# Kernel tuning notes

Measured on AMD Instinct MI355X. Metric: run time of the kernel, lower is better.

## Reference

```python
import jax, jax.numpy as jnp
import numpy as np

N, D, E = 8192, 768, 262144
DI, DS, DCONV, DTR = 1536, 16, 4, 48  # d_inner=2*768, d_state, d_conv, dt_rank=ceil(768/16)


def setup_inputs() -> dict:
    key = jax.random.key(0)
    ks = jax.random.split(key, 12)
    s = 0.02
    return {
        "node_feats": jax.random.normal(ks[0], (N, D), jnp.float32),
        "timestamps": jax.random.randint(ks[1], (N,), 0, 1_000_000, dtype=jnp.int32),
        "edge_index": jax.random.randint(ks[2], (2, E), 0, N, dtype=jnp.int32),
        "W_in": jax.random.normal(ks[3], (D, 2 * DI), jnp.float32) * s,
        "conv_w": jax.random.normal(ks[4], (DI, DCONV), jnp.float32) * s,
        "conv_b": jnp.zeros((DI,), jnp.float32),
        "W_xproj": jax.random.normal(ks[5], (DI, DTR + 2 * DS), jnp.float32) * s,
        "W_dt": jax.random.normal(ks[6], (DTR, DI), jnp.float32) * s,
        "b_dt": jnp.zeros((DI,), jnp.float32),
        "A_log": jnp.log(jnp.broadcast_to(jnp.arange(1, DS + 1, dtype=jnp.float32), (DI, DS))),
        "D_param": jnp.ones((DI,), jnp.float32),
        "W_out": jax.random.normal(ks[7], (DI, D), jnp.float32) * s,
        "Wg": jax.random.normal(ks[8], (3, D, D), jnp.float32) * s,
        "bg": jnp.zeros((3, D), jnp.float32),
        "W_c": jax.random.normal(ks[9], (D, 1), jnp.float32) * s,
        "b_c": jnp.zeros((1,), jnp.float32),
    }


def _mamba(x, W_in, conv_w, conv_b, W_xproj, W_dt, b_dt, A_log, D_param, W_out):
    # x: [L, D]
    L = x.shape[0]
    xz = x @ W_in                      # [L, 2*DI]
    xi, z = xz[:, :DI], xz[:, DI:]
    # causal depthwise conv1d, kernel DCONV
    xp = jnp.pad(xi, ((DCONV - 1, 0), (0, 0)))
    xc = conv_b
    for k in range(DCONV):
        xc = xc + xp[k:k + L] * conv_w[:, k]
    u = jax.nn.silu(xc)                # [L, DI]
    dbc = u @ W_xproj                  # [L, DTR+2*DS]
    delta = jax.nn.softplus(dbc[:, :DTR] @ W_dt + b_dt)  # [L, DI]
    B = dbc[:, DTR:DTR + DS]           # [L, DS]
    C = dbc[:, DTR + DS:]              # [L, DS]
    A = -jnp.exp(A_log)                # [DI, DS]

    def step(h, inp):
        dt, Bt, Ct, ut = inp
        dA = jnp.exp(dt[:, None] * A)                    # [DI, DS]
        h = h * dA + (dt * ut)[:, None] * Bt[None, :]    # [DI, DS]
        return h, (h * Ct[None, :]).sum(-1)              # y_t: [DI]

    h0 = jnp.zeros((DI, DS), x.dtype)
    _, y = jax.lax.scan(step, h0, (delta, B, C, u))      # [L, DI]
    y = (y + u * D_param) * jax.nn.silu(z)
    return y @ W_out                   # [L, D]


def reference(node_feats, timestamps, edge_index, W_in, conv_w, conv_b,
              W_xproj, W_dt, b_dt, A_log, D_param, W_out, Wg, bg, W_c, b_c):
    src, dst = edge_index[0], edge_index[1]
    # degree norms (DGL GraphConv norm='both', clamp min 1)
    ones = jnp.ones((E,), node_feats.dtype)
    out_deg = jnp.clip(jax.ops.segment_sum(ones, src, num_segments=N), 1.0)
    in_deg = jnp.clip(jax.ops.segment_sum(ones, dst, num_segments=N), 1.0)
    norm_s = out_deg ** -0.5
    norm_d = in_deg ** -0.5

    sorted_idx = jnp.argsort(timestamps)
    seq = node_feats[sorted_idx]
    h = _mamba(seq, W_in, conv_w, conv_b, W_xproj, W_dt, b_dt, A_log, D_param, W_out)
    # NOTE: original code feeds sorted-order features to GCN without unsorting (replicated).
    for i in range(3):
        x = h * norm_s[:, None]
        m = jax.ops.segment_sum(x[src], dst, num_segments=N) * norm_d[:, None]
        h = jax.nn.gelu(m @ Wg[i] + bg[i], approximate=False)
    causal = jax.nn.sigmoid(h @ W_c + b_c).squeeze(-1)   # [N]
    graph_feat = h.mean(axis=0)                          # [D]
    return graph_feat, causal, causal > 0.7
```

## Files before the change

kernel.cpp:

```cpp
#include <hip/hip_runtime.h>
#include <math.h>

#define NN 8192
#define DF 768
#define NE_ 262144
#define DIM 1536
#define DSN 16
#define NCH 128
#define CL  64
#define CT  64

typedef short short8 __attribute__((ext_vector_type(8)));
typedef float f32x4 __attribute__((ext_vector_type(4)));
typedef unsigned short us4 __attribute__((ext_vector_type(4)));

__device__ __forceinline__ float bf2f(unsigned short u){
  unsigned int v = ((unsigned int)u) << 16; float f; __builtin_memcpy(&f, &v, 4); return f;
}
__device__ __forceinline__ unsigned short f2bf(float f){
  unsigned int x; __builtin_memcpy(&x, &f, 4);
  x += 0x7fffu + ((x >> 16) & 1u);
  return (unsigned short)(x >> 16);
}
#define EXP2RAW(x) __builtin_amdgcn_exp2f(x)
#define LOG2E 1.44269504088896f
#define LN2   0.69314718055995f
#define H8SCALE 64.f
__device__ __forceinline__ float sigmoidf_(float x){
  return 1.f/(1.f + EXP2RAW(-x*LOG2E));
}
__device__ __forceinline__ float softplusf_(float v){
  if (v > 20.f) return v;
  return LN2 * __log2f(1.f + EXP2RAW(v*LOG2E));
}

__device__ __forceinline__ unsigned char f2fp8(float v){
  float y = v * H8SCALE;
#if __has_builtin(__builtin_amdgcn_cvt_pk_fp8_f32)
  return (unsigned char)(__builtin_amdgcn_cvt_pk_fp8_f32(y, y, 0, false) & 0xff);
#else
  unsigned int u; __builtin_memcpy(&u, &y, 4);
  unsigned char s = (unsigned char)((u >> 24) & 0x80);
  float a = fabsf(y);
  if (a >= 448.f) return (unsigned char)(s | 0x7E);
  if (a < 0x1p-10f) return s;
  unsigned int ab = u & 0x7fffffffu;
  int ef = (int)(ab >> 23) - 127;
  int qe = ef - 3; if (qe < -9) qe = -9;
  float q; { unsigned int qb = (unsigned int)(qe + 127) << 23; __builtin_memcpy(&q, &qb, 4); }
  float n = rintf(a / q);
  float m = n * q;
  unsigned int mb; __builtin_memcpy(&mb, &m, 4);
  int E = (int)(mb >> 23) - 127 + 7;
  unsigned char out;
  if (E <= 0) out = (unsigned char)rintf(m * 512.f);
  else        out = (unsigned char)((E << 3) | ((mb >> 20) & 7));
  return (unsigned char)(s | out);
#endif
}
__device__ __forceinline__ float fp8bits(unsigned int b){
  unsigned int t = ((b & 0x80u) << 24) | ((b & 0x7fu) << 20);
  float f; __builtin_memcpy(&f, &t, 4); return f;
}

__device__ __forceinline__ void gl_lds16(const unsigned short* g, unsigned short* l){
  __builtin_amdgcn_global_load_lds(
      (const __attribute__((address_space(1))) unsigned int*)g,
      (__attribute__((address_space(3))) unsigned int*)l,
      16, 0, 0);
}

__global__ __launch_bounds__(256) void k_prep(
    const float* __restrict__ W_in, const float* __restrict__ W_xproj,
    const float* __restrict__ W_dt, const float* __restrict__ W_out,
    const float* __restrict__ Wg,
    unsigned short* __restrict__ WinT, unsigned short* __restrict__ WxT,
    unsigned short* __restrict__ WdtT, unsigned short* __restrict__ WoutT,
    unsigned short* __restrict__ WgT,
    int* __restrict__ pos, int* __restrict__ degS, float* __restrict__ outv)
{
  int b = blockIdx.x;
  int tid = threadIdx.x;
  if (b >= 1368){
    if (b < 1400)       pos[(b-1368)*256 + tid] = 0;
    else if (b < 1464)  degS[(b-1400)*256 + tid] = 0;
    else { outv[tid] = 0.f; outv[256+tid] = 0.f; outv[512+tid] = 0.f; }
    return;
  }
  const float* in; unsigned short* out; int K, N, Kp, Np, kt, nt;
  if (b < 576){        in = W_in;    out = WinT;  K = 768;  N = 3072; Kp = 768;  Np = 3072;
                       kt = b / 48;  nt = b % 48; }
  else if (b < 624){   int l = b - 576;
                       in = W_xproj; out = WxT;   K = 1536; N = 80;   Kp = 1536; Np = 128;
                       kt = l >> 1;  nt = l & 1; }
  else if (b < 648){   int l = b - 624;
                       in = W_dt;    out = WdtT;  K = 48;   N = 1536; Kp = 64;   Np = 1536;
                       kt = 0;       nt = l; }
  else if (b < 936){   int l = b - 648;
                       in = W_out;   out = WoutT; K = 1536; N = 768;  Kp = 1536; Np = 768;
                       kt = l / 12;  nt = l % 12; }
  else {               int l = b - 936;
                       int g = l / 144; int r = l % 144;
                       in = Wg + (size_t)g*768*768; out = WgT + (size_t)g*768*768;
                       K = 768; N = 768; Kp = 768; Np = 768;
                       kt = r / 12;  nt = r % 12; }
  int k0 = kt*64, n0 = nt*64;
  __shared__ float tl[64][65];
  int ln = tid & 63;
  int lk = tid >> 6;
  #pragma unroll
  for (int kk = lk; kk < 64; kk += 4){
    int gk = k0 + kk, gn = n0 + ln;
    float v = (gk < K && gn < N) ? in[(size_t)gk*N + gn] : 0.f;
    tl[kk][ln] = v;
  }
  __syncthreads();
  #pragma unroll
  for (int nn = lk; nn < 64; nn += 4){
    int gn2 = n0 + nn, gk2 = k0 + ln;
    if (gn2 < Np && gk2 < Kp)
      out[(size_t)gn2*Kp + gk2] = f2bf(tl[ln][nn]);
  }
}

__global__ __launch_bounds__(256) void k_rank_deg(const int* __restrict__ ts, int* __restrict__ pos,
                                                  const int* __restrict__ esrc, const int* __restrict__ edst,
                                                  int* __restrict__ degS, int* __restrict__ degD){
  int b = blockIdx.x;
  if (b < 1024){
    __shared__ int sT[256];
    int ic = b & 31, jc = b >> 5;
    int i = ic*256 + threadIdx.x;
    int my = ts[i];
    int c0 = jc*256;
    sT[threadIdx.x] = ts[c0 + threadIdx.x];
    __syncthreads();
    int r = 0;
    #pragma unroll 8
    for (int j = 0; j < 256; j++){
      int t = sT[j]; int jj = c0 + j;
      r += (t < my || (t == my && jj < i)) ? 1 : 0;
    }
    atomicAdd(&pos[i], r);
  } else {
    int e = (b-1024)*256 + threadIdx.x;
    atomicAdd(&degS[esrc[e]], 1); atomicAdd(&degD[edst[e]], 1);
  }
}

__global__ __launch_bounds__(1024) void k_graphfix(const int* __restrict__ degS, const int* __restrict__ degD,
                                                   float* __restrict__ normS, float* __restrict__ normD,
                                                   int* __restrict__ row_ptr, int* __restrict__ cursor){
  int b = blockIdx.x;
  int tid = threadIdx.x;
  if (b < 8){
    int i = b*1024 + tid;
    normS[i] = rsqrtf(fmaxf((float)degS[i], 1.f));
    normD[i] = rsqrtf(fmaxf((float)degD[i], 1.f));
    return;
  }
  __shared__ int sp[1024];
  int base = tid*8;
  int loc[8]; int s = 0;
  #pragma unroll
  for (int j = 0; j < 8; j++){ loc[j] = degD[base+j]; s += loc[j]; }
  sp[tid] = s; __syncthreads();
  for (int o = 1; o < 1024; o <<= 1){
    int v = (tid >= o) ? sp[tid-o] : 0; __syncthreads();
    sp[tid] += v; __syncthreads();
  }
  int run = sp[tid] - s;
  #pragma unroll
  for (int j = 0; j < 8; j++){ row_ptr[base+j] = run; cursor[base+j] = run; run += loc[j]; }
  if (tid == 1023) row_ptr[NN] = sp[1023];
}

__global__ __launch_bounds__(256) void k_scatter(const float* __restrict__ nf, const int* __restrict__ pos,
                                                 unsigned short* __restrict__ seq,
                                                 const int* __restrict__ esrc, const int* __restrict__ edst,
                                                 int* __restrict__ cursor, int* __restrict__ csr_src){
  int b = blockIdx.x;
  if (b < NN){
    int p = pos[b];
    const float* src = nf + (size_t)b*DF;
    unsigned short* dst = seq + (size_t)p*DF;
    for (int j = threadIdx.x; j < DF/4; j += 256){
      f32x4 v = *(const f32x4*)&src[j*4];
      us4 o = { f2bf(v.x), f2bf(v.y), f2bf(v.z), f2bf(v.w) };
      *(us4*)&dst[j*4] = o;
    }
  } else {
    int e = (b-NN)*256 + threadIdx.x;
    int d = edst[e];
    int p = atomicAdd(&cursor[d], 1);
    csr_src[p] = esrc[e];
  }
}

template<int EPI>
__global__ __launch_bounds__(256) void k_gemm(
    const unsigned short* __restrict__ A, const unsigned short* __restrict__ B,
    int N, int K, int lda, int ldb,
    float* __restrict__ outF, int ldoF,
    unsigned short* __restrict__ outB, int ldoB,
    const float* __restrict__ bias,
    unsigned short* __restrict__ out2,
    unsigned char* __restrict__ outQ,
    const float* __restrict__ nrmS)
{
  __shared__ unsigned short sA[2][128*32];
  __shared__ unsigned short sB[2][128*32];
  int tid = threadIdx.x;
  int tnc = N >> 7;
  int nwg = gridDim.x;
  int bid = blockIdx.x;
  int swz = (nwg & 7) ? bid : ((bid & 7)*(nwg >> 3) + (bid >> 3));
  int bm = (swz / tnc) << 7;
  int bn = (swz % tnc) << 7;
  int wv = tid >> 6, lane = tid & 63;
  int wm = wv >> 1, wn = wv & 1;
  int l15 = lane & 15, l4 = lane >> 4;

  f32x4 acc[4][4];
  #pragma unroll
  for (int i = 0; i < 4; i++)
    #pragma unroll
    for (int j = 0; j < 4; j++)
      acc[i][j] = (f32x4){0.f,0.f,0.f,0.f};

  int r0 = (wv*2)*16 + (lane >> 2);
  int r1 = r0 + 16;
  int cc = (lane & 3)*8;
  const unsigned short* gA0 = A + (size_t)(bm + r0)*lda + cc;
  const unsigned short* gA1 = A + (size_t)(bm + r1)*lda + cc;
  const unsigned short* gB0 = B + (size_t)(bn + r0)*ldb + cc;
  const unsigned short* gB1 = B + (size_t)(bn + r1)*ldb + cc;
  unsigned short* lA0 = &sA[0][(size_t)(wv*2)*512];
  unsigned short* lA1 = &sA[1][(size_t)(wv*2)*512];
  unsigned short* lB0 = &sB[0][(size_t)(wv*2)*512];
  unsigned short* lB1 = &sB[1][(size_t)(wv*2)*512];

  for (int k0 = 0; k0 < K; k0 += 64){
    __syncthreads();
    gl_lds16(gA0 + k0,      lA0);
    gl_lds16(gA1 + k0,      lA0 + 512);
    gl_lds16(gA0 + k0 + 32, lA1);
    gl_lds16(gA1 + k0 + 32, lA1 + 512);
    gl_lds16(gB0 + k0,      lB0);
    gl_lds16(gB1 + k0,      lB0 + 512);
    gl_lds16(gB0 + k0 + 32, lB1);
    gl_lds16(gB1 + k0 + 32, lB1 + 512);
    __syncthreads();
    #pragma unroll
    for (int h = 0; h < 2; h++){
      short8 af[4], bf_[4];
      #pragma unroll
      for (int i = 0; i < 4; i++){
        af[i]  = *(const short8*)&sA[h][(wm*64 + i*16 + l15)*32 + l4*8];
        bf_[i] = *(const short8*)&sB[h][(wn*64 + i*16 + l15)*32 + l4*8];
      }
      #pragma unroll
      for (int i = 0; i < 4; i++)
        #pragma unroll
        for (int j = 0; j < 4; j++)
          acc[i][j] = __builtin_amdgcn_mfma_f32_16x16x32_bf16(af[i], bf_[j], acc[i][j], 0, 0, 0);
    }
  }

  #pragma unroll
  for (int i = 0; i < 4; i++)
    #pragma unroll
    for (int j = 0; j < 4; j++)
      #pragma unroll
      for (int rr = 0; rr < 4; rr++){
        int row = bm + wm*64 + i*16 + l4*4 + rr;
        int col = bn + wn*64 + j*16 + l15;
        float v = acc[i][j][rr];
        if (EPI == 0){
          outB[(size_t)row*ldoB + col] = f2bf(v);
        } else if (EPI == 1){
          outF[(size_t)row*ldoF + col] = v;
          if (col < 64) out2[(size_t)row*64 + col] = (col < 48) ? f2bf(v) : (unsigned short)0;
        } else if (EPI == 2){
          outB[(size_t)row*ldoB + col] = f2bf(softplusf_(v + bias[col]));
        } else if (EPI == 3){
          v += bias[col];
          float g = 0.5f*v*(1.f + erff(v*0.70710678118f));
          outB[(size_t)row*ldoB + col] = f2bf(g);
        } else if (EPI == 4){
          v += bias[col];
          float g = 0.5f*v*(1.f + erff(v*0.70710678118f));
          outQ[(size_t)row*ldoB + col] = f2fp8(g * nrmS[row]);
        } else {
          outQ[(size_t)row*ldoB + col] = f2fp8(v * nrmS[row]);
        }
      }
}

__global__ __launch_bounds__(256) void k_conv_silu(const unsigned short* __restrict__ xz,
                                                   const float* __restrict__ conv_w,
                                                   const float* __restrict__ conv_b,
                                                   unsigned short* __restrict__ u){
  int c = blockIdx.x*256 + threadIdx.x;
  int t0 = blockIdx.y*CT;
  float w0 = conv_w[c*4], w1 = conv_w[c*4+1], w2 = conv_w[c*4+2], w3 = conv_w[c*4+3];
  float bb = conv_b[c];
  const unsigned short* xp = xz + c;
  float x0 = (t0 >= 3) ? bf2f(xp[(size_t)(t0-3)*3072]) : 0.f;
  float x1 = (t0 >= 2) ? bf2f(xp[(size_t)(t0-2)*3072]) : 0.f;
  float x2 = (t0 >= 1) ? bf2f(xp[(size_t)(t0-1)*3072]) : 0.f;
  unsigned short* up = u + (size_t)t0*DIM + c;
  for (int r0 = 0; r0 < CT; r0 += 8){
    unsigned short xb[8];
    #pragma unroll
    for (int j = 0; j < 8; j++) xb[j] = xp[(size_t)(t0+r0+j)*3072];
    #pragma unroll
    for (int j = 0; j < 8; j++){
      float x3 = bf2f(xb[j]);
      float acc = bb + x0*w0 + x1*w1 + x2*w2 + x3*w3;
      up[(r0+j)*DIM] = f2bf(acc * sigmoidf_(acc));
      x0 = x1; x1 = x2; x2 = x3;
    }
  }
}

__device__ __forceinline__ void pow_tree(float e1, float dA[16]){
  float e2 = e1*e1, e4 = e2*e2, e8 = e4*e4;
  dA[0]=e1;      dA[1]=e2;      dA[2]=e2*e1;   dA[3]=e4;
  dA[4]=e4*e1;   dA[5]=e4*e2;   dA[6]=e4*dA[2];dA[7]=e8;
  dA[8]=e8*e1;   dA[9]=e8*e2;   dA[10]=e8*dA[2];dA[11]=e8*e4;
  dA[12]=e8*dA[4];dA[13]=e8*dA[5];dA[14]=e8*dA[6];dA[15]=e8*e8;
}

__global__ __launch_bounds__(256) void k_scanA(
    const unsigned short* __restrict__ delta, const unsigned short* __restrict__ u,
    const float* __restrict__ dbc, const float* __restrict__ A_log,
    const float* __restrict__ D_param,
    float* __restrict__ hend, float* __restrict__ aprod,
    unsigned short* __restrict__ ylocal)
{
  __shared__ float sBC[CL][32];
  int tid = threadIdx.x;
  int c = blockIdx.x*256 + tid;
  int k = blockIdx.y;
  float al2[16];
  #pragma unroll
  for (int s = 0; s < 16; s++) al2[s] = -expf(A_log[(size_t)c*16 + s]) * LOG2E;
  bool fast = true;
  #pragma unroll
  for (int s = 1; s < 16; s++)
    fast = fast && (fabsf(al2[s] - (float)(s+1)*al2[0]) <= 1e-4f*fabsf(al2[s]));
  float Dc = D_param[c];
  float h[16];
  #pragma unroll
  for (int s = 0; s < 16; s++) h[s] = 0.f;
  float sdt = 0.f;
  for (int idx = tid; idx < CL*32; idx += 256){
    int t = idx >> 5, j = idx & 31;
    sBC[t][j] = dbc[(size_t)(k*CL + t)*128 + 48 + j];
  }
  __syncthreads();
  const unsigned short* dp = delta + (size_t)k*CL*DIM + c;
  const unsigned short* up = u + (size_t)k*CL*DIM + c;
  unsigned short* yp = ylocal + (size_t)k*CL*DIM + c;
  if (fast){
    for (int t0 = 0; t0 < CL; t0 += 8){
      unsigned short dtb[8], uub[8];
      #pragma unroll
      for (int j = 0; j < 8; j++){
        dtb[j] = dp[(t0+j)*DIM];
        uub[j] = up[(t0+j)*DIM];
      }
      #pragma unroll
      for (int j = 0; j < 8; j++){
        int t = t0 + j;
        float dt = bf2f(dtb[j]), uu = bf2f(uub[j]);
        f32x4 Bv[4], Cv[4];
        #pragma unroll
        for (int q = 0; q < 4; q++){
          Bv[q] = *(const f32x4*)&sBC[t][q*4];
          Cv[q] = *(const f32x4*)&sBC[t][16 + q*4];
        }
        float dtu = dt*uu;
        sdt += dt;
        float dA[16];
        pow_tree(EXP2RAW(dt*al2[0]), dA);
        float ap[4] = {0.f,0.f,0.f,0.f};
        #pragma unroll
        for (int s = 0; s < 16; s++){
          h[s] = h[s]*dA[s] + dtu*Bv[s>>2][s&3];
          ap[s>>2] += h[s]*Cv[s>>2][s&3];
        }
        float accv = (ap[0]+ap[1]) + (ap[2]+ap[3]);
        yp[t*DIM] = f2bf(accv + uu*Dc);
      }
    }
  } else {
    unsigned short dtn = dp[0], uun = up[0];
    #pragma unroll 2
    for (int t = 0; t < CL; t++){
      float dt = bf2f(dtn), uu = bf2f(uun);
      int tn = (t+1 < CL) ? t+1 : t;
      dtn = dp[tn*DIM]; uun = up[tn*DIM];
      f32x4 Bv[4], Cv[4];
      #pragma unroll
      for (int q = 0; q < 4; q++){
        Bv[q] = *(const f32x4*)&sBC[t][q*4];
        Cv[q] = *(const f32x4*)&sBC[t][16 + q*4];
      }
      float dtu = dt*uu;
      sdt += dt;
      float ap[4] = {0.f,0.f,0.f,0.f};
      #pragma unroll
      for (int s = 0; s < 16; s++){
        float dA = EXP2RAW(dt*al2[s]);
        h[s] = h[s]*dA + dtu*Bv[s>>2][s&3];
        ap[s>>2] += h[s]*Cv[s>>2][s&3];
      }
      float accv = (ap[0]+ap[1]) + (ap[2]+ap[3]);
      yp[t*DIM] = f2bf(accv + uu*Dc);
    }
  }
  size_t base = ((size_t)k*DIM + c)*16;
  #pragma unroll
  for (int s = 0; s < 16; s += 4){
    *(f32x4*)&hend[base+s]  = (f32x4){h[s],h[s+1],h[s+2],h[s+3]};
    *(f32x4*)&aprod[base+s] = (f32x4){EXP2RAW(al2[s]*sdt),EXP2RAW(al2[s+1]*sdt),
                                      EXP2RAW(al2[s+2]*sdt),EXP2RAW(al2[s+3]*sdt)};
  }
}

__global__ __launch_bounds__(256) void k_scanB(float* __restrict__ hend, const float* __restrict__ aprod){
  int i = blockIdx.x*256 + threadIdx.x;
  float H = 0.f;
  for (int k0 = 0; k0 < NCH; k0 += 8){
    float e[8], ap[8];
    #pragma unroll
    for (int j = 0; j < 8; j++){
      size_t o = (size_t)(k0+j)*DIM*16 + i;
      e[j] = hend[o]; ap[j] = aprod[o];
    }
    #pragma unroll
    for (int j = 0; j < 8; j++){
      size_t o = (size_t)(k0+j)*DIM*16 + i;
      hend[o] = H;
      H = e[j] + ap[j]*H;
    }
  }
}

__global__ __launch_bounds__(256) void k_scanCorr(
    const unsigned short* __restrict__ delta, const unsigned short* __restrict__ xz,
    const float* __restrict__ dbc, const float* __restrict__ A_log,
    const float* __restrict__ hin, unsigned short* __restrict__ y)
{
  __shared__ float sC[CL][16];
  int tid = threadIdx.x;
  int c = blockIdx.x*256 + tid;
  int k = blockIdx.y;
  float al2[16];
  #pragma unroll
  for (int s = 0; s < 16; s++) al2[s] = -expf(A_log[(size_t)c*16 + s]) * LOG2E;
  bool fast = true;
  #pragma unroll
  for (int s = 1; s < 16; s++)
    fast = fast && (fabsf(al2[s] - (float)(s+1)*al2[0]) <= 1e-4f*fabsf(al2[s]));
  float alSlow = al2[0];
  #pragma unroll
  for (int s = 1; s < 16; s++) alSlow = fmaxf(alSlow, al2[s]);
  float Hin[16];
  size_t base = ((size_t)k*DIM + c)*16;
  #pragma unroll
  for (int s = 0; s < 16; s += 4){
    f32x4 v = *(const f32x4*)&hin[base+s];
    Hin[s] = v.x; Hin[s+1] = v.y; Hin[s+2] = v.z; Hin[s+3] = v.w;
  }
  for (int idx = tid; idx < CL*16; idx += 256){
    int t = idx >> 4, j = idx & 15;
    sC[t][j] = dbc[(size_t)(k*CL + t)*128 + 64 + j];
  }
  __syncthreads();
  const unsigned short* dp = delta + (size_t)k*CL*DIM + c;
  const unsigned short* zp = xz + (size_t)k*CL*3072 + 1536 + c;
  unsigned short* yp = y + (size_t)k*CL*DIM + c;
  float cum = 0.f;
  int t = 0;
  if (fast){
    bool done = false;
    for (int t0 = 0; t0 < CL && !done; t0 += 8){
      unsigned short dtb[8], zzb[8], ylb[8];
      #pragma unroll
      for (int j = 0; j < 8; j++){
        dtb[j] = dp[(t0+j)*DIM];
        zzb[j] = zp[(t0+j)*3072];
        ylb[j] = yp[(t0+j)*DIM];
      }
      #pragma unroll
      for (int j = 0; j < 8; j++){
        float dt = bf2f(dtb[j]);
        cum += dt;
        float e1 = EXP2RAW(cum*al2[0]);
        if (e1 < 0x1p-33f){ t = t0 + j; done = true; break; }
        float dA[16];
        pow_tree(e1, dA);
        f32x4 Cv[4];
        #pragma unroll
        for (int q = 0; q < 4; q++) Cv[q] = *(const f32x4*)&sC[t0+j][q*4];
        float ap[4] = {0.f,0.f,0.f,0.f};
        #pragma unroll
        for (int s = 0; s < 16; s++)
          ap[s>>2] += Hin[s]*dA[s]*Cv[s>>2][s&3];
        float corr = (ap[0]+ap[1]) + (ap[2]+ap[3]);
        float yl = bf2f(ylb[j]);
        float zz = bf2f(zzb[j]);
        yp[(t0+j)*DIM] = f2bf((yl + corr) * (zz * sigmoidf_(zz)));
      }
      if (!done) t = t0 + 8;
    }
  } else {
    for (; t < CL; t++){
      float dt = bf2f(dp[t*DIM]);
      cum += dt;
      if (EXP2RAW(cum*alSlow) < 0x1p-33f) break;
      f32x4 Cv[4];
      #pragma unroll
      for (int q = 0; q < 4; q++) Cv[q] = *(const f32x4*)&sC[t][q*4];
      float ap[4] = {0.f,0.f,0.f,0.f};
      #pragma unroll
      for (int s = 0; s < 16; s++)
        ap[s>>2] += Hin[s]*EXP2RAW(cum*al2[s])*Cv[s>>2][s&3];
      float corr = (ap[0]+ap[1]) + (ap[2]+ap[3]);
      float yl = bf2f(yp[t*DIM]);
      float zz = bf2f(zp[t*3072]);
      float yv = (yl + corr) * (zz * sigmoidf_(zz));
      yp[t*DIM] = f2bf(yv);
    }
  }
  for (; t + 7 < CL; t += 8){
    unsigned short zzb[8], ylb[8];
    #pragma unroll
    for (int j = 0; j < 8; j++){
      ylb[j] = yp[(t+j)*DIM];
      zzb[j] = zp[(t+j)*3072];
    }
    #pragma unroll
    for (int j = 0; j < 8; j++){
      float yl = bf2f(ylb[j]);
      float zz = bf2f(zzb[j]);
      yp[(t+j)*DIM] = f2bf(yl * (zz * sigmoidf_(zz)));
    }
  }
  for (; t < CL; t++){
    float yl = bf2f(yp[t*DIM]);
    float zz = bf2f(zp[t*3072]);
    yp[t*DIM] = f2bf(yl * (zz * sigmoidf_(zz)));
  }
}

__global__ __launch_bounds__(192) void k_aggregate(
    const unsigned char* __restrict__ hq, const int* __restrict__ row_ptr,
    const int* __restrict__ csr_src, const float* __restrict__ normD,
    unsigned short* __restrict__ m)
{
  int d = blockIdx.x; int tid = threadIdx.x;
  int e0 = row_ptr[d], e1 = row_ptr[d+1];
  float a0 = 0.f, a1 = 0.f, a2 = 0.f, a3 = 0.f;
#if __has_builtin(__builtin_amdgcn_cvt_f32_fp8)
  int e = e0;
  for (; e + 7 < e1; e += 8){
    int sx[8];
    #pragma unroll
    for (int j = 0; j < 8; j++) sx[j] = csr_src[e+j];
    unsigned int w[8];
    #pragma unroll
    for (int j = 0; j < 8; j++) w[j] = *((const unsigned int*)(hq + (size_t)sx[j]*DF) + tid);
    a0 += (__builtin_amdgcn_cvt_f32_fp8(w[0], 0) + __builtin_amdgcn_cvt_f32_fp8(w[1], 0))
        + (__builtin_amdgcn_cvt_f32_fp8(w[2], 0) + __builtin_amdgcn_cvt_f32_fp8(w[3], 0));
    a1 += (__builtin_amdgcn_cvt_f32_fp8(w[0], 1) + __builtin_amdgcn_cvt_f32_fp8(w[1], 1))
        + (__builtin_amdgcn_cvt_f32_fp8(w[2], 1) + __builtin_amdgcn_cvt_f32_fp8(w[3], 1));
    a2 += (__builtin_amdgcn_cvt_f32_fp8(w[0], 2) + __builtin_amdgcn_cvt_f32_fp8(w[1], 2))
        + (__builtin_amdgcn_cvt_f32_fp8(w[2], 2) + __builtin_amdgcn_cvt_f32_fp8(w[3], 2));
    a3 += (__builtin_amdgcn_cvt_f32_fp8(w[0], 3) + __builtin_amdgcn_cvt_f32_fp8(w[1], 3))
        + (__builtin_amdgcn_cvt_f32_fp8(w[2], 3) + __builtin_amdgcn_cvt_f32_fp8(w[3], 3));
    a0 += (__builtin_amdgcn_cvt_f32_fp8(w[4], 0) + __builtin_amdgcn_cvt_f32_fp8(w[5], 0))
        + (__builtin_amdgcn_cvt_f32_fp8(w[6], 0) + __builtin_amdgcn_cvt_f32_fp8(w[7], 0));
    a1 += (__builtin_amdgcn_cvt_f32_fp8(w[4], 1) + __builtin_amdgcn_cvt_f32_fp8(w[5], 1))
        + (__builtin_amdgcn_cvt_f32_fp8(w[6], 1) + __builtin_amdgcn_cvt_f32_fp8(w[7], 1));
    a2 += (__builtin_amdgcn_cvt_f32_fp8(w[4], 2) + __builtin_amdgcn_cvt_f32_fp8(w[5], 2))
        + (__builtin_amdgcn_cvt_f32_fp8(w[6], 2) + __builtin_amdgcn_cvt_f32_fp8(w[7], 2));
    a3 += (__builtin_amdgcn_cvt_f32_fp8(w[4], 3) + __builtin_amdgcn_cvt_f32_fp8(w[5], 3))
        + (__builtin_amdgcn_cvt_f32_fp8(w[6], 3) + __builtin_amdgcn_cvt_f32_fp8(w[7], 3));
  }
  for (; e + 3 < e1; e += 4){
    int s0 = csr_src[e],   s1 = csr_src[e+1];
    int s2 = csr_src[e+2], s3 = csr_src[e+3];
    unsigned int w0 = *((const unsigned int*)(hq + (size_t)s0*DF) + tid);
    unsigned int w1 = *((const unsigned int*)(hq + (size_t)s1*DF) + tid);
    unsigned int w2 = *((const unsigned int*)(hq + (size_t)s2*DF) + tid);
    unsigned int w3 = *((const unsigned int*)(hq + (size_t)s3*DF) + tid);
    a0 += (__builtin_amdgcn_cvt_f32_fp8(w0, 0) + __builtin_amdgcn_cvt_f32_fp8(w1, 0))
        + (__builtin_amdgcn_cvt_f32_fp8(w2, 0) + __builtin_amdgcn_cvt_f32_fp8(w3, 0));
    a1 += (__builtin_amdgcn_cvt_f32_fp8(w0, 1) + __builtin_amdgcn_cvt_f32_fp8(w1, 1))
        + (__builtin_amdgcn_cvt_f32_fp8(w2, 1) + __builtin_amdgcn_cvt_f32_fp8(w3, 1));
    a2 += (__builtin_amdgcn_cvt_f32_fp8(w0, 2) + __builtin_amdgcn_cvt_f32_fp8(w1, 2))
        + (__builtin_amdgcn_cvt_f32_fp8(w2, 2) + __builtin_amdgcn_cvt_f32_fp8(w3, 2));
    a3 += (__builtin_amdgcn_cvt_f32_fp8(w0, 3) + __builtin_amdgcn_cvt_f32_fp8(w1, 3))
        + (__builtin_amdgcn_cvt_f32_fp8(w2, 3) + __builtin_amdgcn_cvt_f32_fp8(w3, 3));
  }
  for (; e < e1; e++){
    int s0 = csr_src[e];
    unsigned int w0 = *((const unsigned int*)(hq + (size_t)s0*DF) + tid);
    a0 += __builtin_amdgcn_cvt_f32_fp8(w0, 0);
    a1 += __builtin_amdgcn_cvt_f32_fp8(w0, 1);
    a2 += __builtin_amdgcn_cvt_f32_fp8(w0, 2);
    a3 += __builtin_amdgcn_cvt_f32_fp8(w0, 3);
  }
  float nd = normD[d] * (1.f/H8SCALE);
#else
  for (int e = e0; e < e1; e++){
    int sI = csr_src[e];
    unsigned int w = *((const unsigned int*)(hq + (size_t)sI*DF) + tid);
    a0 += fp8bits(w & 255u);
    a1 += fp8bits((w >> 8) & 255u);
    a2 += fp8bits((w >> 16) & 255u);
    a3 += fp8bits(w >> 24);
  }
  float nd = normD[d] * 0x1p+114f;
#endif
  uint2 o;
  o.x = (unsigned int)f2bf(a0*nd) | ((unsigned int)f2bf(a1*nd) << 16);
  o.y = (unsigned int)f2bf(a2*nd) | ((unsigned int)f2bf(a3*nd) << 16);
  *((uint2*)(m + (size_t)d*DF) + tid) = o;
}

__global__ __launch_bounds__(256) void k_final(const unsigned short* __restrict__ h,
                                               const float* __restrict__ W_c,
                                               const float* __restrict__ b_c,
                                               float* __restrict__ out){
  int b = blockIdx.x;
  if (b < 2048){
    int wv = threadIdx.x >> 6, lane = threadIdx.x & 63;
    int r = b*4 + wv;
    float s = 0.f;
    #pragma unroll
    for (int j = 0; j < 12; j++){
      int cidx = lane + 64*j;
      s += bf2f(h[(size_t)r*DF + cidx]) * W_c[cidx];
    }
    s += __shfl_xor(s, 32); s += __shfl_xor(s, 16); s += __shfl_xor(s, 8);
    s += __shfl_xor(s, 4);  s += __shfl_xor(s, 2);  s += __shfl_xor(s, 1);
    if (lane == 0){
      float a = s + b_c[0];
      float cz = 1.f/(1.f + expf(-a));
      out[DF + r] = cz;
      out[DF + NN + r] = (cz > 0.7f) ? 1.f : 0.f;
    }
  } else {
    int g = b - 2048;
    int col = (g % 3)*256 + threadIdx.x;
    int r0 = (g / 3)*32;
    float s = 0.f;
    for (int rb = 0; rb < 32; rb += 8){
      unsigned short hb[8];
      #pragma unroll
      for (int j = 0; j < 8; j++) hb[j] = h[(size_t)(r0+rb+j)*DF + col];
      #pragma unroll
      for (int j = 0; j < 8; j++) s += bf2f(hb[j]);
    }
    atomicAdd(&out[col], s * (1.f/8192.f));
  }
}

extern "C" void kernel_launch(void* const* d_in, const int* in_sizes, int n_in,
                              void* d_out, int out_size, void* d_ws, size_t ws_size,
                              hipStream_t stream) {
  const float* node_feats = (const float*)d_in[0];
  const int*   timestamps = (const int*)d_in[1];
  const int*   ei         = (const int*)d_in[2];
  const int*   e_src = ei;
  const int*   e_dst = ei + NE_;
  const float* W_in    = (const float*)d_in[3];
  const float* conv_w  = (const float*)d_in[4];
  const float* conv_b  = (const float*)d_in[5];
  const float* W_xproj = (const float*)d_in[6];
  const float* W_dt    = (const float*)d_in[7];
  const float* b_dt    = (const float*)d_in[8];
  const float* A_log   = (const float*)d_in[9];
  const float* D_param = (const float*)d_in[10];
  const float* W_out   = (const float*)d_in[11];
  const float* Wg      = (const float*)d_in[12];
  const float* bg      = (const float*)d_in[13];
  const float* W_c     = (const float*)d_in[14];
  const float* b_c     = (const float*)d_in[15];
  float* out = (float*)d_out;

  char* ws = (char*)d_ws;
  size_t off = 0;
  auto alloc = [&](size_t bytes) -> char* {
    char* p = ws + off; off += (bytes + 255) & ~(size_t)255; return p;
  };
  unsigned short* WinT   = (unsigned short*)alloc((size_t)3072*768*2);
  unsigned short* WxT    = (unsigned short*)alloc((size_t)128*1536*2);
  unsigned short* WdtT   = (unsigned short*)alloc((size_t)1536*64*2);
  unsigned short* WoutT  = (unsigned short*)alloc((size_t)768*1536*2);
  unsigned short* WgT    = (unsigned short*)alloc((size_t)3*768*768*2);
  unsigned short* seq    = (unsigned short*)alloc((size_t)NN*DF*2);
  unsigned short* xz     = (unsigned short*)alloc((size_t)NN*3072*2);
  unsigned short* ubuf   = (unsigned short*)alloc((size_t)NN*DIM*2);
  float*          dbc    = (float*)alloc((size_t)NN*128*4);
  unsigned short* dt48   = (unsigned short*)alloc((size_t)NN*64*2);
  unsigned short* deltaB = (unsigned short*)alloc((size_t)NN*DIM*2);
  unsigned short* ybuf   = (unsigned short*)alloc((size_t)NN*DIM*2);
  unsigned short* hbuf   = (unsigned short*)alloc((size_t)NN*DF*2);
  unsigned short* mbuf   = (unsigned short*)alloc((size_t)NN*DF*2);
  unsigned char*  hq     = (unsigned char*)alloc((size_t)NN*DF);
  int*   pos    = (int*)alloc((size_t)NN*4);
  int*   degS   = (int*)alloc((size_t)2*NN*4);
  int*   degD   = degS + NN;
  float* normS  = (float*)alloc((size_t)NN*4);
  float* normD  = (float*)alloc((size_t)NN*4);
  int*   rowp   = (int*)alloc((size_t)(NN+1)*4);
  int*   cursor = (int*)alloc((size_t)NN*4);
  int*   csr    = (int*)alloc((size_t)NE_*4);

  float* hend  = (float*)seq;
  float* aprod = (float*)mbuf;

  k_prep<<<1465, 256, 0, stream>>>(W_in, W_xproj, W_dt, W_out, Wg,
                                   WinT, WxT, WdtT, WoutT, WgT,
                                   pos, degS, out);
  k_rank_deg<<<2048, 256, 0, stream>>>(timestamps, pos, e_src, e_dst, degS, degD);
  k_graphfix<<<9, 1024, 0, stream>>>(degS, degD, normS, normD, rowp, cursor);
  k_scatter<<<NN + 1024, 256, 0, stream>>>(node_feats, pos, seq, e_src, e_dst, cursor, csr);

  k_gemm<0><<<64*24, 256, 0, stream>>>(seq, WinT, 3072, 768, 768, 768,
                                       nullptr, 0, xz, 3072, nullptr, nullptr, nullptr, nullptr);
  k_conv_silu<<<dim3(6, NN/CT), 256, 0, stream>>>(xz, conv_w, conv_b, ubuf);
  k_gemm<1><<<64*1, 256, 0, stream>>>(ubuf, WxT, 128, 1536, 1536, 1536,
                                      dbc, 128, nullptr, 0, nullptr, dt48, nullptr, nullptr);
  k_gemm<2><<<64*12, 256, 0, stream>>>(dt48, WdtT, 1536, 64, 64, 64,
                                       nullptr, 0, deltaB, 1536, b_dt, nullptr, nullptr, nullptr);
  k_scanA<<<dim3(DIM/256, NCH), 256, 0, stream>>>(deltaB, ubuf, dbc, A_log, D_param, hend, aprod, ybuf);
  k_scanB<<<96, 256, 0, stream>>>(hend, aprod);
  k_scanCorr<<<dim3(DIM/256, NCH), 256, 0, stream>>>(deltaB, xz, dbc, A_log, hend, ybuf);
  k_gemm<5><<<64*6, 256, 0, stream>>>(ybuf, WoutT, 768, 1536, 1536, 1536,
                                      nullptr, 0, nullptr, 768, nullptr, nullptr, hq, normS);
  k_aggregate<<<NN, 192, 0, stream>>>(hq, rowp, csr, normD, mbuf);
  k_gemm<4><<<64*6, 256, 0, stream>>>(mbuf, WgT, 768, 768, 768, 768,
                                      nullptr, 0, nullptr, 768, bg, nullptr, hq, normS);
  k_aggregate<<<NN, 192, 0, stream>>>(hq, rowp, csr, normD, mbuf);
  k_gemm<4><<<64*6, 256, 0, stream>>>(mbuf, WgT + (size_t)768*768, 768, 768, 768, 768,
                                      nullptr, 0, nullptr, 768, bg + 768, nullptr, hq, normS);
  k_aggregate<<<NN, 192, 0, stream>>>(hq, rowp, csr, normD, mbuf);
  k_gemm<3><<<64*6, 256, 0, stream>>>(mbuf, WgT + (size_t)2*768*768, 768, 768, 768, 768,
                                      nullptr, 0, hbuf, 768, bg + 2*768, nullptr, nullptr, nullptr);
  k_final<<<2816, 256, 0, stream>>>(hbuf, W_c, b_c, out);
}
```

Baseline: 452.9 us.

## Double-buffer GEMM LDS tiles to overlap global loads with MFMA compute

The GEMM main loop now uses the two LDS halves as a ping-pong buffer over 32-wide K steps. It issues the global-to-LDS loads for the next slice before computing on the current one, where the old loop loaded both halves and then computed. This aims to hide global load latency behind MFMA work. In exchange it runs twice as many iterations, each with a barrier, and does half as much MFMA work per iteration. Correctness depends on the direct-to-LDS loads being complete at the single barrier each step.

```diff
diff --git a/kernel.cpp b/kernel.cpp
--- a/kernel.cpp
+++ b/kernel.cpp
@@ -235,36 +235,39 @@
   const unsigned short* gA1 = A + (size_t)(bm + r1)*lda + cc;
   const unsigned short* gB0 = B + (size_t)(bn + r0)*ldb + cc;
   const unsigned short* gB1 = B + (size_t)(bn + r1)*ldb + cc;
-  unsigned short* lA0 = &sA[0][(size_t)(wv*2)*512];
-  unsigned short* lA1 = &sA[1][(size_t)(wv*2)*512];
-  unsigned short* lB0 = &sB[0][(size_t)(wv*2)*512];
-  unsigned short* lB1 = &sB[1][(size_t)(wv*2)*512];
-
-  for (int k0 = 0; k0 < K; k0 += 64){
+  unsigned short* bufA[2] = { &sA[0][(size_t)(wv*2)*512], &sA[1][(size_t)(wv*2)*512] };
+  unsigned short* bufB[2] = { &sB[0][(size_t)(wv*2)*512], &sB[1][(size_t)(wv*2)*512] };
+
+  gl_lds16(gA0, bufA[0]);
+  gl_lds16(gA1, bufA[0] + 512);
+  gl_lds16(gB0, bufB[0]);
+  gl_lds16(gB1, bufB[0] + 512);
+  __syncthreads();
+
+  int nk = K >> 5;
+  int cur = 0;
+  for (int ks = 0; ks < nk; ks++){
+    int nxt = cur ^ 1;
+    if (ks + 1 < nk){
+      int kc = (ks + 1) << 5;
+      gl_lds16(gA0 + kc, bufA[nxt]);
+      gl_lds16(gA1 + kc, bufA[nxt] + 512);
+      gl_lds16(gB0 + kc, bufB[nxt]);
+      gl_lds16(gB1 + kc, bufB[nxt] + 512);
+    }
+    short8 af[4], bf_[4];
+    #pragma unroll
+    for (int i = 0; i < 4; i++){
+      af[i]  = *(const short8*)&sA[cur][(wm*64 + i*16 + l15)*32 + l4*8];
+      bf_[i] = *(const short8*)&sB[cur][(wn*64 + i*16 + l15)*32 + l4*8];
+    }
+    #pragma unroll
+    for (int i = 0; i < 4; i++)
+      #pragma unroll
+      for (int j = 0; j < 4; j++)
+        acc[i][j] = __builtin_amdgcn_mfma_f32_16x16x32_bf16(af[i], bf_[j], acc[i][j], 0, 0, 0);
     __syncthreads();
-    gl_lds16(gA0 + k0,      lA0);
-    gl_lds16(gA1 + k0,      lA0 + 512);
-    gl_lds16(gA0 + k0 + 32, lA1);
-    gl_lds16(gA1 + k0 + 32, lA1 + 512);
-    gl_lds16(gB0 + k0,      lB0);
-    gl_lds16(gB1 + k0,      lB0 + 512);
-    gl_lds16(gB0 + k0 + 32, lB1);
-    gl_lds16(gB1 + k0 + 32, lB1 + 512);
-    __syncthreads();
-    #pragma unroll
-    for (int h = 0; h < 2; h++){
-      short8 af[4], bf_[4];
-      #pragma unroll
-      for (int i = 0; i < 4; i++){
-        af[i]  = *(const short8*)&sA[h][(wm*64 + i*16 + l15)*32 + l4*8];
-        bf_[i] = *(const short8*)&sB[h][(wn*64 + i*16 + l15)*32 + l4*8];
-      }
-      #pragma unroll
-      for (int i = 0; i < 4; i++)
-        #pragma unroll
-        for (int j = 0; j < 4; j++)
-          acc[i][j] = __builtin_amdgcn_mfma_f32_16x16x32_bf16(af[i], bf_[j], acc[i][j], 0, 0, 0);
-    }
+    cur = nxt;
   }
 
   #pragma unroll
```

After: 440.9 us, median of 2. -2.6%, faster.
